# Kernel optimization log

Hardware: AMD Instinct MI355X
Metric: run time of the kernel (lower is better)

## Reference

```python
import jax, jax.numpy as jnp
import numpy as np

SQRT3 = 3.0 ** 0.5
MAX_RADIUS = 5.0
NUM_BASIS = 10
NUM_NEIGHBORS = 15.0
# e3nn soft_one_hot_linspace 'smooth_finite' prefactor: 1.14136 * e^2
SMOOTH_C = 1.14136 * float(np.exp(2.0))


def _sus(x):
    # smooth compactly-supported bump helper: exp(-1/x) for x>0 else 0
    return jnp.where(x > 0.0, jnp.exp(-1.0 / jnp.where(x > 0.0, x, 1.0)), 0.0)


def _soft_one_hot(x):
    # e3nn soft_one_hot_linspace(start=0, end=5, number=10, basis='smooth_finite', cutoff=True)
    values = jnp.linspace(0.0, MAX_RADIUS, NUM_BASIS + 2)[1:-1]  # interior knots
    step = MAX_RADIUS / (NUM_BASIS + 1)
    diff = (x[:, None] - values) / step  # [E, 10]
    return SMOOTH_C * _sus(diff + 1.0) * _sus(1.0 - diff)


def _sh_l1(v, normalize):
    # spherical harmonics up to lmax=1, 'component' normalization.
    # e3nn l=1 component ordering is (y, z, x), each scaled by sqrt(3).
    if normalize:
        v = v / (jnp.linalg.norm(v, axis=-1, keepdims=True) + 1e-9)
    x, y, z = v[..., 0], v[..., 1], v[..., 2]
    return jnp.stack([jnp.ones_like(x), SQRT3 * y, SQRT3 * z, SQRT3 * x], axis=-1)


def setup_inputs() -> dict:
    key = jax.random.key(0)
    ks = jax.random.split(key, 12)
    N, E, G, Fin, D, L, A, H = 100000, 800000, 64, 16, 32, 3, 4, 64
    pos = jax.random.normal(ks[0], (N, 3), jnp.float32) * 1.5
    x = jax.random.normal(ks[1], (N, Fin), jnp.float32)
    orientation = jax.random.uniform(ks[2], (G, 2), jnp.float32)
    edge_src = jax.random.randint(ks[3], (E,), 0, N)
    edge_dst = jax.random.randint(ks[4], (E,), 0, N)
    batch = jnp.sort(jax.random.randint(ks[5], (N,), 0, G))
    W_embed = jax.random.normal(ks[6], (Fin, D), jnp.float32)
    W_tp = jax.random.normal(ks[7], (L, D, A, D), jnp.float32)
    W_fc1 = jax.random.normal(ks[8], (L, NUM_BASIS, H), jnp.float32)
    W_fc2 = jax.random.normal(ks[9], (L, H, 1), jnp.float32)
    W_dec = jax.random.normal(ks[10], (D, A), jnp.float32)
    return {"pos": pos, "x": x, "orientation": orientation, "W_embed": W_embed,
            "W_tp": W_tp, "W_fc1": W_fc1, "W_fc2": W_fc2, "W_dec": W_dec,
            "edge_src": edge_src, "edge_dst": edge_dst, "batch": batch}


def reference(pos, x, orientation, W_embed, W_tp, W_fc1, W_fc2, W_dec,
              edge_src, edge_dst, batch):
    N = x.shape[0]
    G = orientation.shape[0]
    D = W_embed.shape[1]
    A = W_tp.shape[2]
    H = W_fc1.shape[2]

    edge_vec = pos[edge_src] - pos[edge_dst]            # [E, 3]
    edge_len = jnp.linalg.norm(edge_vec, axis=-1)       # [E]
    edge_attr = _sh_l1(edge_vec, True)                  # [E, 4]
    edge_len_emb = _soft_one_hot(edge_len) * (NUM_BASIS ** 0.5)  # [E, 10]

    h = x @ W_embed  # embedding o3.Linear -> [N, D]
    tp_norm = 1.0 / float(np.sqrt(D * A))
    fc1_norm = 1.0 / float(np.sqrt(NUM_BASIS))
    fc2_norm = 1.0 / float(np.sqrt(H))
    agg_norm = 1.0 / float(np.sqrt(NUM_NEIGHBORS))

    for l in range(W_tp.shape[0]):  # fixed small layer count
        h_src = h[edge_src]  # gather [E, D]
        # fully-connected tensor product (bilinear): contract node features with
        # weights first to keep the big intermediate at [E, A, D]
        t = jnp.einsum('ei,iak->eak', h_src, W_tp[l])
        ang = jnp.einsum('eak,ea->ek', t, edge_attr) * tp_norm  # [E, D]
        hid = jax.nn.silu(edge_len_emb @ W_fc1[l] * fc1_norm)   # [E, 64]
        rad = hid @ W_fc2[l] * fc2_norm                          # [E, 1]
        msg = ang * rad                                          # [E, D]
        agg = jax.ops.segment_sum(msg, edge_dst, num_segments=N)
        h = h + agg * agg_norm  # residual

    # graph mean pooling
    gsum = jax.ops.segment_sum(h, batch, num_segments=G)
    cnt = jax.ops.segment_sum(jnp.ones((N,), jnp.float32), batch, num_segments=G)
    graph = gsum / jnp.maximum(cnt, 1.0)[:, None]  # [G, D]

    sh_coeffs = graph @ W_dec  # decoder o3.Linear -> [G, 4]
    theta, phi = orientation[..., 0], orientation[..., 1]
    q = jnp.stack([jnp.sin(theta) * jnp.cos(phi),
                   jnp.sin(theta) * jnp.sin(phi),
                   jnp.cos(theta)], axis=-1)  # unit vectors [G, 3]
    sh_q = _sh_l1(q, False)
    return (sh_coeffs * sh_q).sum(axis=-1)  # [G]
```

## Files before the change

kernel.cpp:

```cpp
#include <hip/hip_runtime.h>


constexpr int Dk  = 32;
constexpr int Ak  = 4;
constexpr int Hk  = 64;
constexpr int NBk = 10;
constexpr int Lk  = 3;
constexpr int FinK = 16;
constexpr int TAB = 8192;

__device__ __forceinline__ float sus(float x) {
    return x > 0.f ? __expf(-1.f / x) : 0.f;
}

__global__ __launch_bounds__(256) void radial_tab_k(
    const float* __restrict__ Wfc1,
    const float* __restrict__ Wfc2,
    float* __restrict__ rtab)
{
    int l = blockIdx.y;
    __shared__ float sW1[NBk * Hk];
    __shared__ float sW2[Hk];
    for (int j = threadIdx.x; j < NBk * Hk; j += blockDim.x) sW1[j] = Wfc1[l * NBk * Hk + j];
    for (int j = threadIdx.x; j < Hk; j += blockDim.x) sW2[j] = Wfc2[l * Hk + j];
    __syncthreads();

    int i = blockIdx.x * blockDim.x + threadIdx.x;
    if (i > TAB) return;
    float len = 5.f * (float)i / (float)TAB;

    const float C_EMB = (float)(1.14136 * 7.3890560989306495);
    float t = len * 2.2f;
    float emb[NBk];
#pragma unroll
    for (int j = 0; j < NBk; j++) {
        float d1 = t - (float)j;
        float d2 = (float)(j + 2) - t;
        emb[j] = C_EMB * sus(d1) * sus(d2);
    }

    const float C_OUT = (float)(0.125 * 0.08838834764831845 * 0.2581988897471611);
    float r = 0.f;
    for (int j = 0; j < Hk; j++) {
        float a = 0.f;
#pragma unroll
        for (int b = 0; b < NBk; b++) a += emb[b] * sW1[b * Hk + j];
        float sg = 1.f / (1.f + __expf(-a));
        r += a * sg * sW2[j];
    }
    rtab[l * (TAB + 1) + i] = r * C_OUT;
}

__global__ __launch_bounds__(256) void edge_pre(
    const float* __restrict__ pos, const int* __restrict__ esrc,
    const int* __restrict__ edst,
    const float* __restrict__ rtab,
    float4* __restrict__ attr,
    float* __restrict__ cfac,
    int E)
{
    int e = blockIdx.x * blockDim.x + threadIdx.x;
    if (e >= E) return;
    int s = esrc[e], d = edst[e];
    float vx = pos[3 * s + 0] - pos[3 * d + 0];
    float vy = pos[3 * s + 1] - pos[3 * d + 1];
    float vz = pos[3 * s + 2] - pos[3 * d + 2];
    float len = sqrtf(vx * vx + vy * vy + vz * vz);
    float inv = 1.f / (len + 1e-9f);
    const float S3 = 1.7320508075688772f;
    attr[e] = make_float4(1.f, S3 * vy * inv, S3 * vz * inv, S3 * vx * inv);

    float xx = fminf(len * ((float)TAB / 5.f), (float)TAB);
    int i = min((int)xx, TAB - 1);
    float f = xx - (float)i;
#pragma unroll
    for (int l = 0; l < Lk; l++) {
        float a = rtab[l * (TAB + 1) + i];
        float b = rtab[l * (TAB + 1) + i + 1];
        cfac[(size_t)l * E + e] = a + (b - a) * f;
    }
}

__global__ __launch_bounds__(256) void embed_k(
    const float* __restrict__ x, const float* __restrict__ We,
    float* __restrict__ h, int N)
{
    __shared__ float sW[FinK * Dk];
    for (int i = threadIdx.x; i < FinK * Dk; i += blockDim.x) sW[i] = We[i];
    __syncthreads();
    int tid = blockIdx.x * blockDim.x + threadIdx.x;
    int n = tid >> 5, k = tid & 31;
    if (n >= N) return;
    float acc = 0.f;
#pragma unroll
    for (int i = 0; i < FinK; i++) acc += x[n * FinK + i] * sW[i * Dk + k];
    h[n * Dk + k] = acc;
}

__global__ __launch_bounds__(256) void tp_gemm(
    const float* __restrict__ h, const float* __restrict__ Wl,
    float* __restrict__ Hp, int N)
{
    int tid = blockIdx.x * blockDim.x + threadIdx.x;
    int n = tid >> 5, k = tid & 31;
    if (n >= N) return;
    float hv = h[(size_t)n * Dk + k];
    float a0 = 0.f, a1 = 0.f, a2 = 0.f, a3 = 0.f;
#pragma unroll
    for (int i = 0; i < Dk; i++) {
        float hb = __shfl(hv, i, 32);
        a0 += hb * Wl[i * 128 + 0 * 32 + k];
        a1 += hb * Wl[i * 128 + 1 * 32 + k];
        a2 += hb * Wl[i * 128 + 2 * 32 + k];
        a3 += hb * Wl[i * 128 + 3 * 32 + k];
    }
    float* o = Hp + (size_t)n * 128;
    o[k] = a0; o[32 + k] = a1; o[64 + k] = a2; o[96 + k] = a3;
}

__global__ __launch_bounds__(256) void edge_scatter(
    const float* __restrict__ Hp, const float4* __restrict__ attr,
    const float* __restrict__ cl, const int* __restrict__ esrc,
    const int* __restrict__ edst, float* __restrict__ h, int E)
{
    int tid = blockIdx.x * blockDim.x + threadIdx.x;
    int e = tid >> 5, k = tid & 31;
    if (e >= E) return;
    int s = esrc[e], d = edst[e];
    float4 a = attr[e];
    float c = cl[e];
    const float* hp = Hp + (size_t)s * 128;
    float v = a.x * hp[k] + a.y * hp[32 + k] + a.z * hp[64 + k] + a.w * hp[96 + k];
    unsafeAtomicAdd(&h[(size_t)d * Dk + k], c * v);
}

constexpr int POOL_NPB = 512;
__global__ __launch_bounds__(256) void pool_k(
    const float* __restrict__ h, const int* __restrict__ batch,
    float* __restrict__ gsum, float* __restrict__ cnt, int N)
{
    int k = threadIdx.x & 31;
    int row = threadIdx.x >> 5;
    int start = blockIdx.x * POOL_NPB;
    int end = min(start + POOL_NPB, N);
    int curg = -1;
    float acc = 0.f, cacc = 0.f;
    for (int n = start + row; n < end; n += 8) {
        int g = batch[n];
        float v = h[(size_t)n * Dk + k];
        if (g != curg) {
            if (curg >= 0) {
                unsafeAtomicAdd(&gsum[curg * Dk + k], acc);
                if (k == 0) unsafeAtomicAdd(&cnt[curg], cacc);
            }
            curg = g; acc = 0.f; cacc = 0.f;
        }
        acc += v; cacc += 1.f;
    }
    if (curg >= 0) {
        unsafeAtomicAdd(&gsum[curg * Dk + k], acc);
        if (k == 0) unsafeAtomicAdd(&cnt[curg], cacc);
    }
}

__global__ __launch_bounds__(64) void final_k(
    const float* __restrict__ gsum, const float* __restrict__ cnt,
    const float* __restrict__ Wdec,
    const float* __restrict__ orient,
    float* __restrict__ out, int G)
{
    int g = blockIdx.x * blockDim.x + threadIdx.x;
    if (g >= G) return;
    float ic = 1.f / fmaxf(cnt[g], 1.f);
    float c0 = 0.f, c1 = 0.f, c2 = 0.f, c3 = 0.f;
#pragma unroll
    for (int i = 0; i < Dk; i++) {
        float gv = gsum[g * Dk + i] * ic;
        c0 += gv * Wdec[i * 4 + 0];
        c1 += gv * Wdec[i * 4 + 1];
        c2 += gv * Wdec[i * 4 + 2];
        c3 += gv * Wdec[i * 4 + 3];
    }
    float th = orient[g * 2 + 0], ph = orient[g * 2 + 1];
    float st = sinf(th), ct = cosf(th), sp = sinf(ph), cp = cosf(ph);
    float qx = st * cp, qy = st * sp, qz = ct;
    const float S3 = 1.7320508075688772f;
    out[g] = c0 + c1 * S3 * qy + c2 * S3 * qz + c3 * S3 * qx;
}

extern "C" void kernel_launch(void* const* d_in, const int* in_sizes, int n_in,
                              void* d_out, int out_size, void* d_ws, size_t ws_size,
                              hipStream_t stream) {
    const float* pos     = (const float*)d_in[0];
    const float* x       = (const float*)d_in[1];
    const float* orient  = (const float*)d_in[2];
    const float* W_embed = (const float*)d_in[3];
    const float* W_tp    = (const float*)d_in[4];
    const float* W_fc1   = (const float*)d_in[5];
    const float* W_fc2   = (const float*)d_in[6];
    const float* W_dec   = (const float*)d_in[7];
    const int*   esrc    = (const int*)d_in[8];
    const int*   edst    = (const int*)d_in[9];
    const int*   batch   = (const int*)d_in[10];

    const int N = in_sizes[0] / 3;
    const int E = in_sizes[8];
    const int G = in_sizes[2] / 2;

    float*  ws   = (float*)d_ws;
    float4* attr = (float4*)ws;
    float*  cfac = ws + (size_t)4 * E;
    float*  h    = cfac + (size_t)3 * E;
    float*  Hp   = h + (size_t)Dk * N;
    float*  gsum = Hp + (size_t)128 * N;
    float*  cnt  = gsum + (size_t)Dk * G;
    float*  rtab = cnt + G;

    hipMemsetAsync(gsum, 0, (size_t)(Dk * G + G) * sizeof(float), stream);

    {
        dim3 grid((TAB + 1 + 255) / 256, Lk);
        radial_tab_k<<<grid, 256, 0, stream>>>(W_fc1, W_fc2, rtab);
    }
    edge_pre<<<(E + 255) / 256, 256, 0, stream>>>(pos, esrc, edst, rtab, attr, cfac, E);
    embed_k<<<(N * 32 + 255) / 256, 256, 0, stream>>>(x, W_embed, h, N);

    for (int l = 0; l < Lk; l++) {
        tp_gemm<<<(N * 32 + 255) / 256, 256, 0, stream>>>(
            h, W_tp + (size_t)l * Dk * Ak * Dk, Hp, N);
        edge_scatter<<<(int)(((size_t)E * 32 + 255) / 256), 256, 0, stream>>>(
            Hp, attr, cfac + (size_t)l * E, esrc, edst, h, E);
    }

    pool_k<<<(N + POOL_NPB - 1) / POOL_NPB, 256, 0, stream>>>(h, batch, gsum, cnt, N);
    final_k<<<(G + 63) / 64, 64, 0, stream>>>(gsum, cnt, W_dec, orient, (float*)d_out, G);
}
```

Measured before the change: 562.8 us.

## Replace atomic edge scatter with CSR gather aggregation and bf16 projected features

Builds a CSR layout by destination (histogram, three-pass scan, atomic slot assignment in edge_pre) so each node's 32-lane group sums its incoming edges in registers and writes h once, with no per-edge float atomics. The per-node projected tensor-product features are also stored as packed bf16, halving the gather traffic. The cost is several extra small kernels for the CSR build, a nondeterministic edge order within each row, and reduced precision in the messages. The W_tp offset is rewritten as an equivalent expression.

```diff
diff --git a/kernel.cpp b/kernel.cpp
--- a/kernel.cpp
+++ b/kernel.cpp
@@ -2,20 +2,26 @@
 
 
 constexpr int Dk  = 32;
-constexpr int Ak  = 4;
 constexpr int Hk  = 64;
 constexpr int NBk = 10;
 constexpr int Lk  = 3;
 constexpr int FinK = 16;
 constexpr int TAB = 8192;
+constexpr int SCB = 256;
 
 __device__ __forceinline__ float sus(float x) {
     return x > 0.f ? __expf(-1.f / x) : 0.f;
 }
 
+__device__ __forceinline__ unsigned pack_bf16_rne(float a, float b) {
+    unsigned ua = __float_as_uint(a), ub = __float_as_uint(b);
+    ua += 0x7FFFu + ((ua >> 16) & 1u);
+    ub += 0x7FFFu + ((ub >> 16) & 1u);
+    return (ua >> 16) | (ub & 0xFFFF0000u);
+}
+
 __global__ __launch_bounds__(256) void radial_tab_k(
-    const float* __restrict__ Wfc1,
-    const float* __restrict__ Wfc2,
+    const float* __restrict__ Wfc1, const float* __restrict__ Wfc2,
     float* __restrict__ rtab)
 {
     int l = blockIdx.y;
@@ -28,7 +34,6 @@
     int i = blockIdx.x * blockDim.x + threadIdx.x;
     if (i > TAB) return;
     float len = 5.f * (float)i / (float)TAB;
-
     const float C_EMB = (float)(1.14136 * 7.3890560989306495);
     float t = len * 2.2f;
     float emb[NBk];
@@ -38,7 +43,6 @@
         float d2 = (float)(j + 2) - t;
         emb[j] = C_EMB * sus(d1) * sus(d2);
     }
-
     const float C_OUT = (float)(0.125 * 0.08838834764831845 * 0.2581988897471611);
     float r = 0.f;
     for (int j = 0; j < Hk; j++) {
@@ -51,13 +55,65 @@
     rtab[l * (TAB + 1) + i] = r * C_OUT;
 }
 
+__global__ __launch_bounds__(256) void hist_k(
+    const int* __restrict__ edst, int* __restrict__ deg, int E)
+{
+    int e = blockIdx.x * blockDim.x + threadIdx.x;
+    if (e < E) atomicAdd(&deg[edst[e]], 1);
+}
+
+__global__ __launch_bounds__(SCB) void scan1_k(
+    const int* __restrict__ deg, int* __restrict__ incl,
+    int* __restrict__ bsum, int N)
+{
+    __shared__ int s[SCB];
+    int g = blockIdx.x * SCB + threadIdx.x;
+    s[threadIdx.x] = (g < N) ? deg[g] : 0;
+    __syncthreads();
+    for (int off = 1; off < SCB; off <<= 1) {
+        int t = (threadIdx.x >= off) ? s[threadIdx.x - off] : 0;
+        __syncthreads();
+        s[threadIdx.x] += t;
+        __syncthreads();
+    }
+    if (g < N) incl[g] = s[threadIdx.x];
+    if (threadIdx.x == SCB - 1) bsum[blockIdx.x] = s[threadIdx.x];
+}
+
+__global__ __launch_bounds__(512) void scan2_k(int* __restrict__ bsum, int nb)
+{
+    __shared__ int s[512];
+    s[threadIdx.x] = (threadIdx.x < nb) ? bsum[threadIdx.x] : 0;
+    __syncthreads();
+    for (int off = 1; off < 512; off <<= 1) {
+        int t = (threadIdx.x >= off) ? s[threadIdx.x - off] : 0;
+        __syncthreads();
+        s[threadIdx.x] += t;
+        __syncthreads();
+    }
+    if (threadIdx.x < nb) bsum[threadIdx.x] = s[threadIdx.x];
+}
+
+__global__ __launch_bounds__(SCB) void scan3_k(
+    const int* __restrict__ deg, const int* __restrict__ incl,
+    const int* __restrict__ bsum, int* __restrict__ row_ptr,
+    int* __restrict__ cur, int N, int E)
+{
+    int g = blockIdx.x * SCB + threadIdx.x;
+    if (g < N) {
+        int off = (blockIdx.x > 0) ? bsum[blockIdx.x - 1] : 0;
+        int excl = incl[g] - deg[g] + off;
+        row_ptr[g] = excl;
+        cur[g] = excl;
+    }
+    if (g == 0) row_ptr[N] = E;
+}
+
 __global__ __launch_bounds__(256) void edge_pre(
     const float* __restrict__ pos, const int* __restrict__ esrc,
-    const int* __restrict__ edst,
-    const float* __restrict__ rtab,
-    float4* __restrict__ attr,
-    float* __restrict__ cfac,
-    int E)
+    const int* __restrict__ edst, const float* __restrict__ rtab,
+    int* __restrict__ cur, int* __restrict__ esrc2,
+    float4* __restrict__ attr2, float* __restrict__ cfac2, int E)
 {
     int e = blockIdx.x * blockDim.x + threadIdx.x;
     if (e >= E) return;
@@ -68,16 +124,19 @@
     float len = sqrtf(vx * vx + vy * vy + vz * vz);
     float inv = 1.f / (len + 1e-9f);
     const float S3 = 1.7320508075688772f;
-    attr[e] = make_float4(1.f, S3 * vy * inv, S3 * vz * inv, S3 * vx * inv);
 
     float xx = fminf(len * ((float)TAB / 5.f), (float)TAB);
     int i = min((int)xx, TAB - 1);
     float f = xx - (float)i;
+
+    int p = atomicAdd(&cur[d], 1);
+    esrc2[p] = s;
+    attr2[p] = make_float4(1.f, S3 * vy * inv, S3 * vz * inv, S3 * vx * inv);
 #pragma unroll
     for (int l = 0; l < Lk; l++) {
         float a = rtab[l * (TAB + 1) + i];
         float b = rtab[l * (TAB + 1) + i + 1];
-        cfac[(size_t)l * E + e] = a + (b - a) * f;
+        cfac2[(size_t)l * E + p] = a + (b - a) * f;
     }
 }
 
@@ -99,7 +158,7 @@
 
 __global__ __launch_bounds__(256) void tp_gemm(
     const float* __restrict__ h, const float* __restrict__ Wl,
-    float* __restrict__ Hp, int N)
+    unsigned* __restrict__ HpU, int N)
 {
     int tid = blockIdx.x * blockDim.x + threadIdx.x;
     int n = tid >> 5, k = tid & 31;
@@ -114,24 +173,34 @@
         a2 += hb * Wl[i * 128 + 2 * 32 + k];
         a3 += hb * Wl[i * 128 + 3 * 32 + k];
     }
-    float* o = Hp + (size_t)n * 128;
-    o[k] = a0; o[32 + k] = a1; o[64 + k] = a2; o[96 + k] = a3;
-}
-
-__global__ __launch_bounds__(256) void edge_scatter(
-    const float* __restrict__ Hp, const float4* __restrict__ attr,
-    const float* __restrict__ cl, const int* __restrict__ esrc,
-    const int* __restrict__ edst, float* __restrict__ h, int E)
+    unsigned* o = HpU + (size_t)n * 64;
+    o[k]      = pack_bf16_rne(a0, a1);
+    o[32 + k] = pack_bf16_rne(a2, a3);
+}
+
+__global__ __launch_bounds__(256) void agg_k(
+    const unsigned* __restrict__ HpU, const float4* __restrict__ attr2,
+    const float* __restrict__ cl, const int* __restrict__ esrc2,
+    const int* __restrict__ row_ptr, float* __restrict__ h, int N)
 {
     int tid = blockIdx.x * blockDim.x + threadIdx.x;
-    int e = tid >> 5, k = tid & 31;
-    if (e >= E) return;
-    int s = esrc[e], d = edst[e];
-    float4 a = attr[e];
-    float c = cl[e];
-    const float* hp = Hp + (size_t)s * 128;
-    float v = a.x * hp[k] + a.y * hp[32 + k] + a.z * hp[64 + k] + a.w * hp[96 + k];
-    unsafeAtomicAdd(&h[(size_t)d * Dk + k], c * v);
+    int n = tid >> 5, k = tid & 31;
+    if (n >= N) return;
+    int r0 = row_ptr[n], r1 = row_ptr[n + 1];
+    float acc = 0.f;
+    for (int i = r0; i < r1; ++i) {
+        int s = esrc2[i];
+        float4 a = attr2[i];
+        float c = cl[i];
+        const unsigned* hp = HpU + (size_t)s * 64;
+        unsigned u01 = hp[k], u23 = hp[32 + k];
+        float h0 = __uint_as_float(u01 << 16);
+        float h1 = __uint_as_float(u01 & 0xFFFF0000u);
+        float h2 = __uint_as_float(u23 << 16);
+        float h3 = __uint_as_float(u23 & 0xFFFF0000u);
+        acc += c * (a.x * h0 + a.y * h1 + a.z * h2 + a.w * h3);
+    }
+    h[(size_t)n * Dk + k] += acc;
 }
 
 constexpr int POOL_NPB = 512;
@@ -165,8 +234,7 @@
 
 __global__ __launch_bounds__(64) void final_k(
     const float* __restrict__ gsum, const float* __restrict__ cnt,
-    const float* __restrict__ Wdec,
-    const float* __restrict__ orient,
+    const float* __restrict__ Wdec, const float* __restrict__ orient,
     float* __restrict__ out, int G)
 {
     int g = blockIdx.x * blockDim.x + threadIdx.x;
@@ -206,30 +274,44 @@
     const int N = in_sizes[0] / 3;
     const int E = in_sizes[8];
     const int G = in_sizes[2] / 2;
-
-    float*  ws   = (float*)d_ws;
-    float4* attr = (float4*)ws;
-    float*  cfac = ws + (size_t)4 * E;
-    float*  h    = cfac + (size_t)3 * E;
-    float*  Hp   = h + (size_t)Dk * N;
-    float*  gsum = Hp + (size_t)128 * N;
-    float*  cnt  = gsum + (size_t)Dk * G;
-    float*  rtab = cnt + G;
-
+    const int NB = (N + SCB - 1) / SCB;
+
+    float*    ws     = (float*)d_ws;
+    float4*   attr2  = (float4*)ws;
+    float*    cfac2  = ws + (size_t)4 * E;
+    float*    h      = cfac2 + (size_t)3 * E;
+    unsigned* HpU    = (unsigned*)(h + (size_t)Dk * N);
+    float*    gsum   = (float*)(HpU + (size_t)64 * N);
+    float*    cnt    = gsum + (size_t)Dk * G;
+    float*    rtab   = cnt + G;
+    int*      esrc2  = (int*)(rtab + 3 * (TAB + 1));
+    int*      deg    = esrc2 + E;
+    int*      incl   = deg + N;
+    int*      row_ptr= incl + N;
+    int*      cur    = row_ptr + (N + 1);
+    int*      bsum   = cur + N;
+
+    hipMemsetAsync(deg, 0, (size_t)N * sizeof(int), stream);
     hipMemsetAsync(gsum, 0, (size_t)(Dk * G + G) * sizeof(float), stream);
 
     {
         dim3 grid((TAB + 1 + 255) / 256, Lk);
         radial_tab_k<<<grid, 256, 0, stream>>>(W_fc1, W_fc2, rtab);
     }
-    edge_pre<<<(E + 255) / 256, 256, 0, stream>>>(pos, esrc, edst, rtab, attr, cfac, E);
+    hist_k<<<(E + 255) / 256, 256, 0, stream>>>(edst, deg, E);
+    scan1_k<<<NB, SCB, 0, stream>>>(deg, incl, bsum, N);
+    scan2_k<<<1, 512, 0, stream>>>(bsum, NB);
+    scan3_k<<<NB, SCB, 0, stream>>>(deg, incl, bsum, row_ptr, cur, N, E);
+
+    edge_pre<<<(E + 255) / 256, 256, 0, stream>>>(
+        pos, esrc, edst, rtab, cur, esrc2, attr2, cfac2, E);
     embed_k<<<(N * 32 + 255) / 256, 256, 0, stream>>>(x, W_embed, h, N);
 
     for (int l = 0; l < Lk; l++) {
         tp_gemm<<<(N * 32 + 255) / 256, 256, 0, stream>>>(
-            h, W_tp + (size_t)l * Dk * Ak * Dk, Hp, N);
-        edge_scatter<<<(int)(((size_t)E * 32 + 255) / 256), 256, 0, stream>>>(
-            Hp, attr, cfac + (size_t)l * E, esrc, edst, h, E);
+            h, W_tp + (size_t)l * 128 * 32 / 32 * 32, HpU, N);
+        agg_k<<<(N * 32 + 255) / 256, 256, 0, stream>>>(
+            HpU, attr2, cfac2 + (size_t)l * E, esrc2, row_ptr, h, N);
     }
 
     pool_k<<<(N + POOL_NPB - 1) / POOL_NPB, 256, 0, stream>>>(h, batch, gsum, cnt, N);
```

After: 571.8 us. No clear change (+1.6%).
